# Performance work log

Hardware: AMD Instinct MI355X
Metric: run time of the kernel (lower is better)

Reference implementation:

```python
import jax, jax.numpy as jnp
import numpy as np

C_DIM = 768
NH = 12
MLP_HIDDEN = 3072


def _ln(x, g, b, eps=1e-5):
    mu = x.mean(-1, keepdims=True)
    var = ((x - mu) ** 2).mean(-1, keepdims=True)
    return (x - mu) / jnp.sqrt(var + eps) * g + b


def _mha(x, Wqkv, nh, scale):
    # x: [N, L, C]; Wqkv: [C, 3C] packed as (3, nh, hd) on output dim
    N, L, C = x.shape
    hd = C // nh
    qkv = (x @ Wqkv).reshape(N, L, 3, nh, hd)
    q, k, v = qkv[:, :, 0], qkv[:, :, 1], qkv[:, :, 2]  # [N, L, nh, hd]
    a = jnp.einsum('nqhd,nkhd->nhqk', q, k) * scale
    a = jax.nn.softmax(a, axis=-1)
    o = jnp.einsum('nhqk,nkhd->nqhd', a, v).reshape(N, L, C)
    return o


def setup_inputs() -> dict:
    key = jax.random.key(0)
    ks = jax.random.split(key, 16)
    B, T, K, C = 4, 16, 196, C_DIM
    s = 0.02
    inp = {
        'x': jax.random.normal(ks[0], (B, 1 + K * T, C), jnp.float32),
        'B': B, 'T': T, 'K': K,
        'ln1_g': jnp.ones((C,)), 'ln1_b': jnp.zeros((C,)),
        'lnt_g': jnp.ones((C,)), 'lnt_b': jnp.zeros((C,)),
        'ln2_g': jnp.ones((C,)), 'ln2_b': jnp.zeros((C,)),
        'lncls_g': jnp.ones((C,)), 'lncls_b': jnp.zeros((C,)),
        'Wqkv_s': jax.random.normal(ks[1], (C, 3 * C)) * s,
        'Wproj_s': jax.random.normal(ks[2], (C, C)) * s,
        'bproj_s': jnp.zeros((C,)),
        'Wqkv4': jax.random.normal(ks[3], (C, 3 * C)) * s,
        'Wqkv8': jax.random.normal(ks[4], (C, 3 * C)) * s,
        'Wqkv16': jax.random.normal(ks[5], (C, 3 * C)) * s,
        'Wp4': jax.random.normal(ks[6], (C, C)) * s, 'bp4': jnp.zeros((C,)),
        'Wp8': jax.random.normal(ks[7], (C, C)) * s, 'bp8': jnp.zeros((C,)),
        'Wp16': jax.random.normal(ks[8], (C, C)) * s, 'bp16': jnp.zeros((C,)),
        'Wtfc': jax.random.normal(ks[9], (C, C)) * s, 'btfc': jnp.zeros((C,)),
        'Wfc1': jax.random.normal(ks[10], (C, MLP_HIDDEN)) * s, 'bfc1': jnp.zeros((MLP_HIDDEN,)),
        'Wfc2': jax.random.normal(ks[11], (MLP_HIDDEN, C)) * s, 'bfc2': jnp.zeros((C,)),
    }
    return inp


def reference(x, B, T, K, ln1_g, ln1_b, lnt_g, lnt_b, ln2_g, ln2_b,
              lncls_g, lncls_b, Wqkv_s, Wproj_s, bproj_s,
              Wqkv4, Wqkv8, Wqkv16, Wp4, bp4, Wp8, bp8, Wp16, bp16,
              Wtfc, btfc, Wfc1, bfc1, Wfc2, bfc2):
    C = x.shape[-1]
    nh = NH
    scale = (C // nh) ** -0.5
    t1, t2 = T // 4, T // 2

    # ---- multi-scale temporal attention (eval mode: all dropout identity) ----
    xt = x[:, 1:, :].reshape(B, K, T, C).reshape(B * K, T, C)
    xt_n = _ln(xt, lnt_g, lnt_b)
    x4 = _mha(xt_n[:, T - t1:], Wqkv4, nh, scale) @ Wp4 + bp4    # [BK, t1, C]
    x8 = _mha(xt_n[:, t2:], Wqkv8, nh, scale) @ Wp8 + bp8        # [BK, t2, C]
    x16 = _mha(xt_n, Wqkv16, nh, scale) @ Wp16 + bp16            # [BK, T, C]
    # windowed fusion of overlapping scales
    x8 = jnp.concatenate([x8[:, :t1], 0.5 * x8[:, t1:] + 0.5 * x4], axis=1)
    x16 = jnp.concatenate([x16[:, :t2], 0.5 * x16[:, t2:] + 0.5 * x8], axis=1)
    res_temp = x16.reshape(B, K * T, C)
    xt_full = res_temp @ Wtfc + btfc + x[:, 1:, :]               # [B, K*T, C]

    # ---- spatial attention with replicated CLS token ----
    init_cls = x[:, 0:1, :]                                      # [B, 1, C]
    cls_rep = jnp.broadcast_to(init_cls, (B, T, C)).reshape(B * T, 1, C)
    xs = xt_full.reshape(B, K, T, C).transpose(0, 2, 1, 3).reshape(B * T, K, C)
    xs = jnp.concatenate([cls_rep, xs], axis=1)                  # [B*T, K+1, C]
    res_spatial = _mha(_ln(xs, ln1_g, ln1_b), Wqkv_s, nh, scale) @ Wproj_s + bproj_s

    # ---- CLS aggregation over time ----
    cls_sp = _ln(res_spatial[:, 0, :].reshape(B, T, C), lncls_g, lncls_b)
    target = cls_sp[:, -1:, :]                                   # [B, 1, C]
    attn2 = jax.nn.softmax(jnp.einsum('bqc,btc->bqt', target, cls_sp), axis=-1)
    cls_sp = attn2 @ cls_sp                                      # [B, 1, C]

    x_s = res_spatial[:, 1:, :].reshape(B, T, K, C).transpose(0, 2, 1, 3).reshape(B, K * T, C)
    x_cat = jnp.concatenate([init_cls, xt_full], axis=1) + jnp.concatenate([cls_sp, x_s], axis=1)

    # ---- MLP residual ----
    h = _ln(x_cat, ln2_g, ln2_b)
    h = jax.nn.gelu(h @ Wfc1 + bfc1, approximate=False) @ Wfc2 + bfc2
    return x_cat + h
```

## Files before the change

kernel.cpp:

```cpp
#include <hip/hip_runtime.h>
#include <hip/hip_bf16.h>
#include <stdint.h>

#define BF16 __hip_bfloat16

typedef __attribute__((ext_vector_type(8))) short short8;
typedef __attribute__((ext_vector_type(2))) short short2v;
typedef __attribute__((ext_vector_type(4))) float floatx4;

typedef const __attribute__((address_space(1))) void* gas_cvp;
typedef __attribute__((address_space(3))) void* las_vp;

__device__ __forceinline__ float bf2f(BF16 v) { return __bfloat162float(v); }
__device__ __forceinline__ BF16 f2bf(float v) { return __float2bfloat16(v); }

__global__ __launch_bounds__(256) void wtrans(const float* __restrict__ W,
                                              BF16* __restrict__ Wt, int K, int N) {
    __shared__ float t[32][33];
    int k0 = blockIdx.x * 32, n0 = blockIdx.y * 32;
    int tx = threadIdx.x & 31, ty = threadIdx.x >> 5;
#pragma unroll
    for (int i = 0; i < 32; i += 8) t[ty + i][tx] = W[(size_t)(k0 + ty + i) * N + n0 + tx];
    __syncthreads();
#pragma unroll
    for (int i = 0; i < 32; i += 8)
        Wt[(size_t)(n0 + ty + i) * K + k0 + tx] = f2bf(t[tx][ty + i]);
}

struct WTJob { const float* src; BF16* dst; int K; int N; int boff; };
struct WTParams { WTJob j[12]; };

__global__ __launch_bounds__(256) void wtrans_all(WTParams P) {
    __shared__ float t[32][33];
    const int bid = blockIdx.x;
    int ji = 0;
#pragma unroll
    for (int i = 1; i < 12; ++i)
        if (bid >= P.j[i].boff) ji = i;
    const float* __restrict__ W = P.j[ji].src;
    BF16* __restrict__ Wt = P.j[ji].dst;
    const int K = P.j[ji].K, N = P.j[ji].N;
    const int lb = bid - P.j[ji].boff;
    const int kb = K >> 5;
    const int k0 = (lb % kb) * 32, n0 = (lb / kb) * 32;
    const int tx = threadIdx.x & 31, ty = threadIdx.x >> 5;
#pragma unroll
    for (int i = 0; i < 32; i += 8) t[ty + i][tx] = W[(size_t)(k0 + ty + i) * N + n0 + tx];
    __syncthreads();
#pragma unroll
    for (int i = 0; i < 32; i += 8)
        Wt[(size_t)(n0 + ty + i) * K + k0 + tx] = f2bf(t[tx][ty + i]);
}

template <int MODE>
__global__ __launch_bounds__(256) void ln_kernel(const float* __restrict__ src0,
                                                 const float* __restrict__ src1,
                                                 const BF16* __restrict__ srcb,
                                                 const float* __restrict__ g,
                                                 const float* __restrict__ bta,
                                                 BF16* __restrict__ dst_bf,
                                                 float* __restrict__ dst_f) {
    const int r = blockIdx.x, tid = threadIdx.x;
    float x0, x1, x2;
    {
        const float* src;
        if (MODE == 0) {
            int b = r / 3136, rr = r - b * 3136;
            src = src0 + ((size_t)b * 3137 + 1 + rr) * 768;
        } else if (MODE == 1) {
            int bt = r / 197, j = r - bt * 197;
            int b = bt >> 4, t = bt & 15;
            if (j == 0) src = src0 + (size_t)b * 3137 * 768;
            else        src = src1 + ((size_t)(b * 3137 + 1) + (size_t)(j - 1) * 16 + t) * 768;
        } else {
            src = src0 + (size_t)r * 768;
        }
        x0 = src[tid]; x1 = src[tid + 256]; x2 = src[tid + 512];
    }
    float s = x0 + x1 + x2;
    float ss = x0 * x0 + x1 * x1 + x2 * x2;
    __shared__ float red[8];
#pragma unroll
    for (int o = 32; o > 0; o >>= 1) { s += __shfl_down(s, o); ss += __shfl_down(ss, o); }
    if ((tid & 63) == 0) { red[tid >> 6] = s; red[4 + (tid >> 6)] = ss; }
    __syncthreads();
    s = red[0] + red[1] + red[2] + red[3];
    ss = red[4] + red[5] + red[6] + red[7];
    const float mu = s * (1.0f / 768.0f);
    const float var = ss * (1.0f / 768.0f) - mu * mu;
    const float rstd = rsqrtf(var + 1e-5f);
#pragma unroll
    for (int i = 0; i < 3; ++i) {
        int c = tid + i * 256;
        float xv = (i == 0) ? x0 : (i == 1) ? x1 : x2;
        float y = (xv - mu) * rstd * g[c] + bta[c];
        dst_bf[(size_t)r * 768 + c] = f2bf(y);
    }
}

template <int AMAP, int OMODE>
__device__ __forceinline__ void gemm_body(BF16* Al, BF16* Bl,
                                          int orig, int nwg, int gx,
                                          const BF16* __restrict__ A,
                                          const BF16* __restrict__ Bt,
                                          const float* __restrict__ bias,
                                          const void* res, void* Cout,
                                          int M, int N, int K) {
    const int tid = threadIdx.x;
    const int lane = tid & 63;
    const int w = tid >> 6;

    const int xcd = orig & 7;
    const int idx = orig >> 3;
    const int q8 = nwg >> 3, r8 = nwg & 7;
    const int wgid = (xcd < r8 ? xcd * (q8 + 1) : r8 * (q8 + 1) + (xcd - r8) * q8) + idx;
    const int bn0 = (wgid % gx) * 128;
    const int bm0 = (wgid / gx) * 128;

    const BF16* gsrc[8];
    BF16* ldst[8];
    const int rin = lane >> 3;
    const int kblk = (lane & 7) ^ rin;
#pragma unroll
    for (int j = 0; j < 8; ++j) {
        int c = w * 8 + j;
        if (c < 16) {
            int gr = bm0 + c * 8 + rin;
            if (gr > M - 1) gr = M - 1;
            if (AMAP == 1) gr = (gr >> 3) * 16 + 8 + (gr & 7);
            if (AMAP == 2) gr = (gr >> 2) * 16 + 12 + (gr & 3);
            gsrc[j] = A + (size_t)gr * K + kblk * 8;
            ldst[j] = Al + c * 512;
        } else {
            int gn = bn0 + (c - 16) * 8 + rin;
            gsrc[j] = Bt + (size_t)gn * K + kblk * 8;
            ldst[j] = Bl + (c - 16) * 512;
        }
    }

    const int wm = (w & 1) * 64;
    const int wn = (w >> 1) * 64;
    const int fr = lane & 15;
    const int fq = lane >> 4;
    const int sw = fr & 7;
    const int o0 = (fq ^ sw) * 8;
    const int o1 = ((fq + 4) ^ sw) * 8;
    const BF16* pa[4];
    const BF16* pb[4];
#pragma unroll
    for (int t = 0; t < 4; ++t) {
        pa[t] = Al + (wm + t * 16 + fr) * 64;
        pb[t] = Bl + (wn + t * 16 + fr) * 64;
    }

    floatx4 acc[4][4];
#pragma unroll
    for (int i = 0; i < 4; ++i)
#pragma unroll
        for (int j = 0; j < 4; ++j) acc[i][j] = (floatx4){0.f, 0.f, 0.f, 0.f};

    for (int k0 = 0; k0 < K; k0 += 64) {
#pragma unroll
        for (int j = 0; j < 8; ++j) {
            __builtin_amdgcn_global_load_lds((gas_cvp)gsrc[j], (las_vp)ldst[j], 16, 0, 0);
            gsrc[j] += 64;
        }
        __syncthreads();
        {
            short8 af[4], bfr[4];
#pragma unroll
            for (int t = 0; t < 4; ++t) {
                af[t] = *(const short8*)(pa[t] + o0);
                bfr[t] = *(const short8*)(pb[t] + o0);
            }
#pragma unroll
            for (int mt = 0; mt < 4; ++mt)
#pragma unroll
                for (int nt = 0; nt < 4; ++nt)
                    acc[mt][nt] = __builtin_amdgcn_mfma_f32_16x16x32_bf16(af[mt], bfr[nt], acc[mt][nt], 0, 0, 0);
#pragma unroll
            for (int t = 0; t < 4; ++t) {
                af[t] = *(const short8*)(pa[t] + o1);
                bfr[t] = *(const short8*)(pb[t] + o1);
            }
#pragma unroll
            for (int mt = 0; mt < 4; ++mt)
#pragma unroll
                for (int nt = 0; nt < 4; ++nt)
                    acc[mt][nt] = __builtin_amdgcn_mfma_f32_16x16x32_bf16(af[mt], bfr[nt], acc[mt][nt], 0, 0, 0);
        }
        __syncthreads();
    }

#pragma unroll
    for (int mt = 0; mt < 4; ++mt) {
#pragma unroll
        for (int nt = 0; nt < 4; ++nt) {
            const int gcol = bn0 + wn + nt * 16 + fr;
#pragma unroll
            for (int r = 0; r < 4; ++r) {
                const int grow = bm0 + wm + mt * 16 + fq * 4 + r;
                if (grow < M) {
                    float v = acc[mt][nt][r];
                    if (OMODE != 0 && OMODE != 8) v += bias[gcol];
                    if (OMODE == 0 || OMODE == 1) {
                        ((BF16*)Cout)[(size_t)grow * N + gcol] = f2bf(v);
                    } else if (OMODE == 2) {
                        int t8 = grow & 7;
                        int rr = (grow >> 3) * 16 + 8 + t8;
                        float w8 = (t8 < 4) ? 0.5f : 0.25f;
                        BF16* R = (BF16*)Cout;
                        size_t o = (size_t)rr * 768 + gcol;
                        R[o] = f2bf(0.5f * bf2f(R[o]) + w8 * v);
                    } else if (OMODE == 3) {
                        int t4 = grow & 3;
                        int rr = (grow >> 2) * 16 + 12 + t4;
                        BF16* R = (BF16*)Cout;
                        size_t o = (size_t)rr * 768 + gcol;
                        R[o] = f2bf(bf2f(R[o]) + 0.25f * v);
                    } else if (OMODE == 4) {
                        int b = grow / 3136;
                        size_t xrow = (size_t)b * 3137 + 1 + (grow - b * 3136);
                        ((float*)Cout)[xrow * 768 + gcol] =
                            v + ((const float*)res)[xrow * 768 + gcol];
                    } else if (OMODE == 6) {
                        float u = v * (0.7978845608f + 0.0356774081f * v * v);
                        v = v / (1.0f + __expf(-2.0f * u));
                        ((BF16*)Cout)[(size_t)grow * N + gcol] = f2bf(v);
                    } else {
                        v += ((const float*)res)[(size_t)grow * N + gcol];
                        ((float*)Cout)[(size_t)grow * N + gcol] = v;
                    }
                }
            }
        }
    }
}

template <int AMAP, int OMODE>
__global__ __launch_bounds__(256) void gemm_bf16(const BF16* __restrict__ A,
                                                 const BF16* __restrict__ Bt,
                                                 const float* __restrict__ bias,
                                                 const void* res,
                                                 void* Cout,
                                                 int M, int N, int K) {
    __shared__ BF16 Al[128 * 64];
    __shared__ BF16 Bl[128 * 64];
    const int gx = gridDim.x;
    const int nwg = gx * (int)gridDim.y;
    const int orig = (int)blockIdx.y * gx + (int)blockIdx.x;
    gemm_body<AMAP, OMODE>(Al, Bl, orig, nwg, gx, A, Bt, bias, res, Cout, M, N, K);
}

template <int AMAP0, int OMODE0, int AMAP1, int OMODE1>
__global__ __launch_bounds__(256) void gemm_dual(
        int nblk0, int gx0,
        const BF16* A0, const BF16* B0, const float* b0, const void* r0, void* C0,
        int M0, int N0, int K0,
        int gx1,
        const BF16* A1, const BF16* B1, const float* b1, const void* r1, void* C1,
        int M1, int N1, int K1) {
    __shared__ BF16 Al[128 * 64];
    __shared__ BF16 Bl[128 * 64];
    const int bid = blockIdx.x;
    if (bid < nblk0)
        gemm_body<AMAP0, OMODE0>(Al, Bl, bid, nblk0, gx0, A0, B0, b0, r0, C0, M0, N0, K0);
    else
        gemm_body<AMAP1, OMODE1>(Al, Bl, bid - nblk0, (int)gridDim.x - nblk0, gx1,
                                 A1, B1, b1, r1, C1, M1, N1, K1);
}

template <int L, int NT>
__global__ __launch_bounds__(NT) void temporal_attn(const BF16* __restrict__ qkv,
                                                    BF16* __restrict__ outp) {
    __shared__ float q[L * 64];
    __shared__ float k[L * 65];
    __shared__ float v[L * 64];
    __shared__ float S[L * L];
    const int bh = blockIdx.x;
    const int b = bh / 12, h = bh % 12;
    const int tid = threadIdx.x;
    const size_t rb = (size_t)b * L;
    for (int idx = tid; idx < L * 64; idx += NT) {
        int i = idx >> 6, d = idx & 63;
        size_t base = (rb + i) * 2304 + h * 64 + d;
        q[i * 64 + d] = bf2f(qkv[base]);
        k[i * 65 + d] = bf2f(qkv[base + 768]);
        v[i * 64 + d] = bf2f(qkv[base + 1536]);
    }
    __syncthreads();
    for (int idx = tid; idx < L * L; idx += NT) {
        int i = idx / L, j = idx % L;
        float a = 0.f;
#pragma unroll
        for (int d = 0; d < 64; ++d) a += q[i * 64 + d] * k[j * 65 + d];
        S[idx] = a * 0.125f;
    }
    __syncthreads();
    if (tid < L) {
        float mx = -1e30f;
        for (int j = 0; j < L; ++j) mx = fmaxf(mx, S[tid * L + j]);
        float sm = 0.f;
        for (int j = 0; j < L; ++j) { float e = __expf(S[tid * L + j] - mx); S[tid * L + j] = e; sm += e; }
        float inv = 1.0f / sm;
        for (int j = 0; j < L; ++j) S[tid * L + j] *= inv;
    }
    __syncthreads();
    for (int idx = tid; idx < L * 64; idx += NT) {
        int i = idx >> 6, d = idx & 63;
        float acc = 0.f;
#pragma unroll
        for (int j = 0; j < L; ++j) acc += S[i * L + j] * v[j * 64 + d];
        outp[(rb + i) * 768 + h * 64 + d] = f2bf(acc);
    }
}

__global__ __launch_bounds__(256) void spatial_attn_mfma(const BF16* __restrict__ qkv,
                                                         BF16* __restrict__ outp) {
    const int bid = blockIdx.x;
    const int qt = bid & 3;
    const int h = (bid >> 2) % 12;
    const int bt = bid / 48;
    const int rowbase = bt * 197;
    __shared__ BF16 KsPl[208 * 72];
    __shared__ BF16 Vt[64 * 232];
    const int tid = threadIdx.x;
    const int lane = tid & 63;
    const int w = tid >> 6;
    const int ln = lane & 15;
    const int quad = lane >> 4;

    for (int it = tid; it < 208 * 8; it += 256) {
        int key = it >> 3, c = it & 7;
        int kc = key < 197 ? key : 196;
        short8 gk = *(const short8*)(qkv + (size_t)(rowbase + kc) * 2304 + 768 + h * 64 + c * 8);
        *(short8*)&KsPl[key * 72 + c * 8] = gk;
    }
    for (int it = tid; it < 112 * 8; it += 256) {
        int p = it >> 3, c = it & 7;
        int kc0 = (2 * p < 197) ? 2 * p : 196;
        int kc1 = (2 * p + 1 < 197) ? 2 * p + 1 : 196;
        short8 a = *(const short8*)(qkv + (size_t)(rowbase + kc0) * 2304 + 1536 + h * 64 + c * 8);
        short8 b = *(const short8*)(qkv + (size_t)(rowbase + kc1) * 2304 + 1536 + h * 64 + c * 8);
#pragma unroll
        for (int e = 0; e < 8; ++e) {
            short2v pr;
            pr[0] = a[e];
            pr[1] = b[e];
            *(short2v*)&Vt[(c * 8 + e) * 232 + 2 * p] = pr;
        }
    }
    __syncthreads();

    const int m0 = qt * 64 + w * 16;
    int qrow = m0 + ln; if (qrow > 196) qrow = 196;
    const BF16* qptr = qkv + (size_t)(rowbase + qrow) * 2304 + h * 64 + quad * 8;
    short8 aq0 = *(const short8*)(qptr);
    short8 aq1 = *(const short8*)(qptr + 32);

    floatx4 sacc[13];
#pragma unroll
    for (int nt = 0; nt < 13; ++nt) sacc[nt] = (floatx4){0.f, 0.f, 0.f, 0.f};
#pragma unroll
    for (int nt = 0; nt < 13; ++nt) {
        const BF16* kb = &KsPl[(nt * 16 + ln) * 72 + quad * 8];
        short8 b0 = *(const short8*)kb;
        short8 b1 = *(const short8*)(kb + 32);
        sacc[nt] = __builtin_amdgcn_mfma_f32_16x16x32_bf16(aq0, b0, sacc[nt], 0, 0, 0);
        sacc[nt] = __builtin_amdgcn_mfma_f32_16x16x32_bf16(aq1, b1, sacc[nt], 0, 0, 0);
    }
    __syncthreads();

#pragma unroll
    for (int r = 0; r < 4; ++r) {
        float mx = -1e30f;
#pragma unroll
        for (int nt = 0; nt < 13; ++nt) {
            float s = sacc[nt][r] * 0.125f;
            sacc[nt][r] = s;
            if (nt * 16 + ln < 197) mx = fmaxf(mx, s);
        }
        mx = fmaxf(mx, __shfl_xor(mx, 1));
        mx = fmaxf(mx, __shfl_xor(mx, 2));
        mx = fmaxf(mx, __shfl_xor(mx, 4));
        mx = fmaxf(mx, __shfl_xor(mx, 8));
        float sum = 0.f;
#pragma unroll
        for (int nt = 0; nt < 13; ++nt) {
            float e = (nt * 16 + ln < 197) ? __expf(sacc[nt][r] - mx) : 0.f;
            sacc[nt][r] = e;
            sum += e;
        }
        sum += __shfl_xor(sum, 1);
        sum += __shfl_xor(sum, 2);
        sum += __shfl_xor(sum, 4);
        sum += __shfl_xor(sum, 8);
        float inv = 1.0f / sum;
#pragma unroll
        for (int nt = 0; nt < 13; ++nt) sacc[nt][r] *= inv;
    }

    BF16* pw = KsPl + w * (16 * 232);
#pragma unroll
    for (int nt = 0; nt < 13; ++nt)
#pragma unroll
        for (int r = 0; r < 4; ++r)
            pw[(quad * 4 + r) * 232 + nt * 16 + ln] = f2bf(sacc[nt][r]);
#pragma unroll
    for (int r = 0; r < 4; ++r)
        pw[(quad * 4 + r) * 232 + 208 + ln] = f2bf(0.f);

    floatx4 oacc[4];
#pragma unroll
    for (int nt = 0; nt < 4; ++nt) oacc[nt] = (floatx4){0.f, 0.f, 0.f, 0.f};
    for (int kb = 0; kb < 7; ++kb) {
        short8 ap = *(const short8*)&pw[ln * 232 + kb * 32 + quad * 8];
#pragma unroll
        for (int nt = 0; nt < 4; ++nt) {
            short8 bv = *(const short8*)&Vt[(nt * 16 + ln) * 232 + kb * 32 + quad * 8];
            oacc[nt] = __builtin_amdgcn_mfma_f32_16x16x32_bf16(ap, bv, oacc[nt], 0, 0, 0);
        }
    }

#pragma unroll
    for (int nt = 0; nt < 4; ++nt) {
        int dim = nt * 16 + ln;
#pragma unroll
        for (int r = 0; r < 4; ++r) {
            int q = m0 + quad * 4 + r;
            if (q < 197)
                outp[(size_t)(rowbase + q) * 768 + h * 64 + dim] = f2bf(oacc[nt][r]);
        }
    }
}

__global__ __launch_bounds__(256) void cls_ln_attn_kernel(const BF16* __restrict__ res_sp,
                                                          const float* __restrict__ g,
                                                          const float* __restrict__ bta,
                                                          float* __restrict__ clsout) {
    const int b = blockIdx.x;
    const int tid = threadIdx.x;
    __shared__ float sLN[16][768];
    __shared__ float red[8];
    __shared__ float dots[16];
    __shared__ float aw[16];

    for (int t = 0; t < 16; ++t) {
        const BF16* src = res_sp + (size_t)((b * 16 + t) * 197) * 768;
        float x0 = bf2f(src[tid]);
        float x1 = bf2f(src[tid + 256]);
        float x2 = bf2f(src[tid + 512]);
        float s = x0 + x1 + x2;
        float ss = x0 * x0 + x1 * x1 + x2 * x2;
#pragma unroll
        for (int o = 32; o > 0; o >>= 1) { s += __shfl_down(s, o); ss += __shfl_down(ss, o); }
        if ((tid & 63) == 0) { red[tid >> 6] = s; red[4 + (tid >> 6)] = ss; }
        __syncthreads();
        s = red[0] + red[1] + red[2] + red[3];
        ss = red[4] + red[5] + red[6] + red[7];
        const float mu = s * (1.0f / 768.0f);
        const float var = ss * (1.0f / 768.0f) - mu * mu;
        const float rstd = rsqrtf(var + 1e-5f);
        sLN[t][tid]       = (x0 - mu) * rstd * g[tid] + bta[tid];
        sLN[t][tid + 256] = (x1 - mu) * rstd * g[tid + 256] + bta[tid + 256];
        sLN[t][tid + 512] = (x2 - mu) * rstd * g[tid + 512] + bta[tid + 512];
        __syncthreads();
    }

    const int t = tid >> 4, l16 = tid & 15;
    float p = 0.f;
    for (int c = l16; c < 768; c += 16) p += sLN[15][c] * sLN[t][c];
#pragma unroll
    for (int o = 8; o > 0; o >>= 1) p += __shfl_down(p, o, 16);
    if (l16 == 0) dots[t] = p;
    __syncthreads();
    if (tid == 0) {
        float mx = -1e30f;
        for (int j = 0; j < 16; ++j) mx = fmaxf(mx, dots[j]);
        float s = 0.f;
        for (int j = 0; j < 16; ++j) { aw[j] = __expf(dots[j] - mx); s += aw[j]; }
        float inv = 1.0f / s;
        for (int j = 0; j < 16; ++j) aw[j] *= inv;
    }
    __syncthreads();
    for (int c = tid; c < 768; c += 256) {
        float acc = 0.f;
#pragma unroll
        for (int j = 0; j < 16; ++j) acc += aw[j] * sLN[j][c];
        clsout[(size_t)b * 768 + c] = acc;
    }
}

__global__ __launch_bounds__(256) void xcat_ln_kernel(const float* __restrict__ x,
                                                      const BF16* __restrict__ res_sp,
                                                      const float* __restrict__ clsout,
                                                      const float* __restrict__ g,
                                                      const float* __restrict__ bta,
                                                      float* outbuf,
                                                      BF16* __restrict__ hln) {
    const int gidx = blockIdx.x;
    const int b = gidx / 3137, j = gidx - b * 3137;
    const int tid = threadIdx.x;
    float v0, v1, v2;
    if (j == 0) {
        const float* xr = x + (size_t)b * 3137 * 768;
        const float* cr = clsout + (size_t)b * 768;
        v0 = xr[tid] + cr[tid];
        v1 = xr[tid + 256] + cr[tid + 256];
        v2 = xr[tid + 512] + cr[tid + 512];
    } else {
        const int p = j - 1, k = p >> 4, t = p & 15;
        const BF16* rs = res_sp + (size_t)((b * 16 + t) * 197 + 1 + k) * 768;
        float* orow = outbuf + (size_t)gidx * 768;
        v0 = orow[tid] + bf2f(rs[tid]);
        v1 = orow[tid + 256] + bf2f(rs[tid + 256]);
        v2 = orow[tid + 512] + bf2f(rs[tid + 512]);
    }
    float* orow = outbuf + (size_t)gidx * 768;
    orow[tid] = v0; orow[tid + 256] = v1; orow[tid + 512] = v2;

    float s = v0 + v1 + v2;
    float ss = v0 * v0 + v1 * v1 + v2 * v2;
    __shared__ float red[8];
#pragma unroll
    for (int o = 32; o > 0; o >>= 1) { s += __shfl_down(s, o); ss += __shfl_down(ss, o); }
    if ((tid & 63) == 0) { red[tid >> 6] = s; red[4 + (tid >> 6)] = ss; }
    __syncthreads();
    s = red[0] + red[1] + red[2] + red[3];
    ss = red[4] + red[5] + red[6] + red[7];
    const float mu = s * (1.0f / 768.0f);
    const float var = ss * (1.0f / 768.0f) - mu * mu;
    const float rstd = rsqrtf(var + 1e-5f);
#pragma unroll
    for (int i = 0; i < 3; ++i) {
        int c = tid + i * 256;
        float xv = (i == 0) ? v0 : (i == 1) ? v1 : v2;
        hln[(size_t)gidx * 768 + c] = f2bf((xv - mu) * rstd * g[c] + bta[c]);
    }
}

extern "C" void kernel_launch(void* const* d_in, const int* in_sizes, int n_in,
                              void* d_out, int out_size, void* d_ws, size_t ws_size,
                              hipStream_t stream) {
    const float* x       = (const float*)d_in[0];
    const float* ln1_g   = (const float*)d_in[4];
    const float* ln1_b   = (const float*)d_in[5];
    const float* lnt_g   = (const float*)d_in[6];
    const float* lnt_b   = (const float*)d_in[7];
    const float* ln2_g   = (const float*)d_in[8];
    const float* ln2_b   = (const float*)d_in[9];
    const float* lncls_g = (const float*)d_in[10];
    const float* lncls_b = (const float*)d_in[11];
    const float* Wqkv_s  = (const float*)d_in[12];
    const float* Wproj_s = (const float*)d_in[13];
    const float* bproj_s = (const float*)d_in[14];
    const float* Wqkv4   = (const float*)d_in[15];
    const float* Wqkv8   = (const float*)d_in[16];
    const float* Wqkv16  = (const float*)d_in[17];
    const float* Wp4     = (const float*)d_in[18];
    const float* bp4     = (const float*)d_in[19];
    const float* Wp8     = (const float*)d_in[20];
    const float* bp8     = (const float*)d_in[21];
    const float* Wp16    = (const float*)d_in[22];
    const float* bp16    = (const float*)d_in[23];
    const float* Wtfc    = (const float*)d_in[24];
    const float* btfc    = (const float*)d_in[25];
    const float* Wfc1    = (const float*)d_in[26];
    const float* bfc1    = (const float*)d_in[27];
    const float* Wfc2    = (const float*)d_in[28];
    const float* bfc2    = (const float*)d_in[29];
    float* out = (float*)d_out;

    const size_t oW0 = 0;
    const size_t oW1 = 4718592;
    const size_t oR1 = 9437184;
    const size_t oR2 = 28803072;
    const size_t oR3 = 48070656;
    const size_t oR4 = 77119488;
    const size_t oCO = 96681984;
    const size_t NEED = 96694272;
    const size_t NEED_BIG = NEED + 29491200;
    if (ws_size < NEED) return;
    char* ws = (char*)d_ws;

    BF16* w0       = (BF16*)(ws + oW0);
    BF16* w1       = (BF16*)(ws + oW1);
    BF16* xtn      = (BF16*)(ws + oR1);
    BF16* atts     = (BF16*)(ws + oR1);
    BF16* hln      = (BF16*)(ws + oR1);
    BF16* res_temp = (BF16*)(ws + oR2);
    BF16* h1       = (BF16*)(ws + oR2);
    BF16* qkv      = (BF16*)(ws + oR3);
    BF16* att      = (BF16*)(ws + oR4);
    BF16* xsn      = (BF16*)(ws + oR4);
    BF16* res_sp   = (BF16*)(ws + oR4);
    float* clsout  = (float*)(ws + oCO);

    const bool big = (ws_size >= NEED_BIG);
    BF16 *tqkv16, *tqkv8, *tqkv4, *tqkvs, *tp16, *tp8, *tp4, *ttfc, *tproj, *tfc1, *tfc2;
    if (big) {
        char* wx = ws + NEED;
        tqkv16 = (BF16*)wx; wx += 3538944;
        tqkv8  = (BF16*)wx; wx += 3538944;
        tqkv4  = (BF16*)wx; wx += 3538944;
        tqkvs  = (BF16*)wx; wx += 3538944;
        tp16   = (BF16*)wx; wx += 1179648;
        tp8    = (BF16*)wx; wx += 1179648;
        tp4    = (BF16*)wx; wx += 1179648;
        ttfc   = (BF16*)wx; wx += 1179648;
        tproj  = (BF16*)wx; wx += 1179648;
        tfc1   = (BF16*)wx; wx += 4718592;
        tfc2   = (BF16*)wx; wx += 4718592;
        WTParams P;
        P.j[0]  = { Wqkv16,                     tqkv16,                     768, 2304,     0 };
        P.j[1]  = { Wqkv8,                      tqkv8,                      768, 2304,  1728 };
        P.j[2]  = { Wqkv4,                      tqkv4,                      768, 2304,  3456 };
        P.j[3]  = { Wqkv_s,                     tqkvs,                      768, 2304,  5184 };
        P.j[4]  = { Wp16,                       tp16,                       768,  768,  6912 };
        P.j[5]  = { Wp8,                        tp8,                        768,  768,  7488 };
        P.j[6]  = { Wp4,                        tp4,                        768,  768,  8064 };
        P.j[7]  = { Wtfc,                       ttfc,                       768,  768,  8640 };
        P.j[8]  = { Wproj_s,                    tproj,                      768,  768,  9216 };
        P.j[9]  = { Wfc1,                       tfc1,                       768, 3072,  9792 };
        P.j[10] = { Wfc2,                       tfc2,                      1536,  768, 12096 };
        P.j[11] = { Wfc2 + (size_t)1536 * 768,  tfc2 + (size_t)768 * 1536, 1536,  768, 13248 };
        wtrans_all<<<14400, 256, 0, stream>>>(P);
    } else {
        tqkv16 = w0; tqkv8 = w0; tqkv4 = w0; tqkvs = w1;
        tp16 = w1; tp8 = w1; tp4 = w1; ttfc = w0; tproj = w0;
        tfc1 = w0; tfc2 = w1;
    }

    ln_kernel<0><<<12544, 256, 0, stream>>>(x, nullptr, nullptr, lnt_g, lnt_b, xtn, nullptr);

    if (!big) wtrans<<<dim3(24, 72), 256, 0, stream>>>(Wqkv16, tqkv16, 768, 2304);
    for (int c = 0; c < 2; ++c) {
        gemm_bf16<0, 0><<<dim3(18, 49), 256, 0, stream>>>(xtn + (size_t)c * 6272 * 768, tqkv16, nullptr, nullptr, qkv, 6272, 2304, 768);
        temporal_attn<16, 256><<<4704, 256, 0, stream>>>(qkv, att + (size_t)c * 6272 * 768);
    }

    if (!big) {
        wtrans<<<dim3(24, 24), 256, 0, stream>>>(Wp16, tp16, 768, 768);
        wtrans<<<dim3(24, 72), 256, 0, stream>>>(Wqkv8, tqkv8, 768, 2304);
    }
    gemm_dual<0, 1, 1, 0><<<588 + 882, 256, 0, stream>>>(
        588, 6, att, tp16, bp16, nullptr, res_temp, 12544, 768, 768,
        18, xtn, tqkv8, nullptr, nullptr, qkv, 6272, 2304, 768);
    temporal_attn<8, 64><<<9408, 64, 0, stream>>>(qkv, att);

    if (!big) {
        wtrans<<<dim3(24, 24), 256, 0, stream>>>(Wp8, tp8, 768, 768);
        wtrans<<<dim3(24, 72), 256, 0, stream>>>(Wqkv4, tqkv4, 768, 2304);
    }
    gemm_dual<0, 2, 2, 0><<<294 + 450, 256, 0, stream>>>(
        294, 6, att, tp8, bp8, nullptr, res_temp, 6272, 768, 768,
        18, xtn, tqkv4, nullptr, nullptr, qkv, 3136, 2304, 768);
    temporal_attn<4, 64><<<9408, 64, 0, stream>>>(qkv, att);

    if (!big) wtrans<<<dim3(24, 24), 256, 0, stream>>>(Wp4, tp4, 768, 768);
    gemm_bf16<0, 3><<<dim3(6, 25), 256, 0, stream>>>(att, tp4, bp4, nullptr, res_temp, 3136, 768, 768);

    if (!big) wtrans<<<dim3(24, 24), 256, 0, stream>>>(Wtfc, ttfc, 768, 768);
    gemm_bf16<0, 4><<<dim3(6, 98), 256, 0, stream>>>(res_temp, ttfc, btfc, x, out, 12544, 768, 768);

    ln_kernel<1><<<12608, 256, 0, stream>>>(x, out, nullptr, ln1_g, ln1_b, xsn, nullptr);
    if (!big) wtrans<<<dim3(24, 72), 256, 0, stream>>>(Wqkv_s, tqkvs, 768, 2304);
    for (int c = 0; c < 2; ++c) {
        gemm_bf16<0, 0><<<dim3(18, 50), 256, 0, stream>>>(xsn + (size_t)c * 6304 * 768, tqkvs, nullptr, nullptr, qkv, 6304, 2304, 768);
        spatial_attn_mfma<<<1536, 256, 0, stream>>>(qkv, atts + (size_t)c * 6304 * 768);
    }
    if (!big) wtrans<<<dim3(24, 24), 256, 0, stream>>>(Wproj_s, tproj, 768, 768);
    gemm_bf16<0, 1><<<dim3(6, 99), 256, 0, stream>>>(atts, tproj, bproj_s, nullptr, res_sp, 12608, 768, 768);

    cls_ln_attn_kernel<<<4, 256, 0, stream>>>(res_sp, lncls_g, lncls_b, clsout);

    xcat_ln_kernel<<<12548, 256, 0, stream>>>(x, res_sp, clsout, ln2_g, ln2_b, out, hln);

    if (!big) {
        wtrans<<<dim3(24, 96), 256, 0, stream>>>(Wfc1, tfc1, 768, 3072);
        wtrans<<<dim3(48, 24), 256, 0, stream>>>(Wfc2, tfc2, 1536, 768);
        wtrans<<<dim3(48, 24), 256, 0, stream>>>(Wfc2 + (size_t)1536 * 768, tfc2 + (size_t)768 * 1536, 1536, 768);
    }

    gemm_bf16<0, 6><<<dim3(12, 99), 256, 0, stream>>>(hln, tfc1, bfc1, nullptr, h1, 12548, 1536, 768);
    gemm_bf16<0, 7><<<dim3(6, 99), 256, 0, stream>>>(h1, tfc2, bfc2, out, out, 12548, 768, 1536);
    gemm_bf16<0, 6><<<dim3(12, 99), 256, 0, stream>>>(hln, tfc1 + (size_t)1536 * 768, bfc1 + 1536, nullptr, h1, 12548, 1536, 768);
    gemm_bf16<0, 8><<<dim3(6, 99), 256, 0, stream>>>(h1, tfc2 + (size_t)768 * 1536, nullptr, out, out, 12548, 768, 1536);
}
```

Before: 942.5 us.

## Co-schedule MLP fc2 first half with fc1 second half; vectorize temporal attention IO

When the workspace is large enough, the MLP's first-half fc2 GEMM and second-half fc1 GEMM are launched as one dual-GEMM kernel, writing the second hidden buffer to a separate workspace region. This removes a launch boundary and lets the two independent GEMMs share the GPU so tail waves overlap. Separately, temporal attention now loads Q/K/V and stores its output in 8-element bf16 vectors instead of scalars. The dual path needs extra workspace and only runs if the harness provides it.

```diff
diff --git a/kernel.cpp b/kernel.cpp
--- a/kernel.cpp
+++ b/kernel.cpp
@@ -281,12 +281,18 @@
     const int b = bh / 12, h = bh % 12;
     const int tid = threadIdx.x;
     const size_t rb = (size_t)b * L;
-    for (int idx = tid; idx < L * 64; idx += NT) {
-        int i = idx >> 6, d = idx & 63;
-        size_t base = (rb + i) * 2304 + h * 64 + d;
-        q[i * 64 + d] = bf2f(qkv[base]);
-        k[i * 65 + d] = bf2f(qkv[base + 768]);
-        v[i * 64 + d] = bf2f(qkv[base + 1536]);
+    for (int idx = tid; idx < L * 8; idx += NT) {
+        int i = idx >> 3, d8 = (idx & 7) * 8;
+        size_t base = (rb + i) * 2304 + h * 64 + d8;
+        short8 qv = *(const short8*)(qkv + base);
+        short8 kv = *(const short8*)(qkv + base + 768);
+        short8 vv = *(const short8*)(qkv + base + 1536);
+#pragma unroll
+        for (int e = 0; e < 8; ++e) {
+            q[i * 64 + d8 + e] = bf2f(((const BF16*)&qv)[e]);
+            k[i * 65 + d8 + e] = bf2f(((const BF16*)&kv)[e]);
+            v[i * 64 + d8 + e] = bf2f(((const BF16*)&vv)[e]);
+        }
     }
     __syncthreads();
     for (int idx = tid; idx < L * L; idx += NT) {
@@ -306,12 +312,21 @@
         for (int j = 0; j < L; ++j) S[tid * L + j] *= inv;
     }
     __syncthreads();
-    for (int idx = tid; idx < L * 64; idx += NT) {
-        int i = idx >> 6, d = idx & 63;
-        float acc = 0.f;
-#pragma unroll
-        for (int j = 0; j < L; ++j) acc += S[i * L + j] * v[j * 64 + d];
-        outp[(rb + i) * 768 + h * 64 + d] = f2bf(acc);
+    for (int idx = tid; idx < L * 8; idx += NT) {
+        int i = idx >> 3, d8 = (idx & 7) * 8;
+        float acc[8];
+#pragma unroll
+        for (int e = 0; e < 8; ++e) acc[e] = 0.f;
+#pragma unroll
+        for (int j = 0; j < L; ++j) {
+            float sv = S[i * L + j];
+#pragma unroll
+            for (int e = 0; e < 8; ++e) acc[e] += sv * v[j * 64 + d8 + e];
+        }
+        short8 ov;
+#pragma unroll
+        for (int e = 0; e < 8; ++e) ((BF16*)&ov)[e] = f2bf(acc[e]);
+        *(short8*)(outp + (rb + i) * 768 + h * 64 + d8) = ov;
     }
 }
 
@@ -580,6 +595,7 @@
     const size_t oCO = 96681984;
     const size_t NEED = 96694272;
     const size_t NEED_BIG = NEED + 29491200;
+    const size_t NEED_C   = NEED_BIG + 38547456;
     if (ws_size < NEED) return;
     char* ws = (char*)d_ws;
 
@@ -597,6 +613,8 @@
     float* clsout  = (float*)(ws + oCO);
 
     const bool big = (ws_size >= NEED_BIG);
+    const bool featC = (ws_size >= NEED_C);
+    BF16* h1b = featC ? (BF16*)(ws + NEED_BIG) : nullptr;
     BF16 *tqkv16, *tqkv8, *tqkv4, *tqkvs, *tp16, *tp8, *tp4, *ttfc, *tproj, *tfc1, *tfc2;
     if (big) {
         char* wx = ws + NEED;
@@ -682,8 +700,16 @@
         wtrans<<<dim3(48, 24), 256, 0, stream>>>(Wfc2 + (size_t)1536 * 768, tfc2 + (size_t)768 * 1536, 1536, 768);
     }
 
-    gemm_bf16<0, 6><<<dim3(12, 99), 256, 0, stream>>>(hln, tfc1, bfc1, nullptr, h1, 12548, 1536, 768);
-    gemm_bf16<0, 7><<<dim3(6, 99), 256, 0, stream>>>(h1, tfc2, bfc2, out, out, 12548, 768, 1536);
-    gemm_bf16<0, 6><<<dim3(12, 99), 256, 0, stream>>>(hln, tfc1 + (size_t)1536 * 768, bfc1 + 1536, nullptr, h1, 12548, 1536, 768);
-    gemm_bf16<0, 8><<<dim3(6, 99), 256, 0, stream>>>(h1, tfc2 + (size_t)768 * 1536, nullptr, out, out, 12548, 768, 1536);
-}
+    if (featC) {
+        gemm_bf16<0, 6><<<dim3(12, 99), 256, 0, stream>>>(hln, tfc1, bfc1, nullptr, h1, 12548, 1536, 768);
+        gemm_dual<0, 7, 0, 6><<<594 + 1188, 256, 0, stream>>>(
+            594, 6, h1, tfc2, bfc2, out, out, 12548, 768, 1536,
+            12, hln, tfc1 + (size_t)1536 * 768, bfc1 + 1536, nullptr, h1b, 12548, 1536, 768);
+        gemm_bf16<0, 8><<<dim3(6, 99), 256, 0, stream>>>(h1b, tfc2 + (size_t)768 * 1536, nullptr, out, out, 12548, 768, 1536);
+    } else {
+        gemm_bf16<0, 6><<<dim3(12, 99), 256, 0, stream>>>(hln, tfc1, bfc1, nullptr, h1, 12548, 1536, 768);
+        gemm_bf16<0, 7><<<dim3(6, 99), 256, 0, stream>>>(h1, tfc2, bfc2, out, out, 12548, 768, 1536);
+        gemm_bf16<0, 6><<<dim3(12, 99), 256, 0, stream>>>(hln, tfc1 + (size_t)1536 * 768, bfc1 + 1536, nullptr, h1, 12548, 1536, 768);
+        gemm_bf16<0, 8><<<dim3(6, 99), 256, 0, stream>>>(h1, tfc2 + (size_t)768 * 1536, nullptr, out, out, 12548, 768, 1536);
+    }
+}
```

After: 926.7 us. Within noise of the previous version (-1.7%).
